# Kernel optimization log

Measured on AMD Instinct MI355X. Metric: run time of the kernel, lower is better.

## Reference

```python
import jax, jax.numpy as jnp
import numpy as np

D = 1024
EPS = 1e-5

def layer_norm(x, g, b):
    m = jnp.mean(x, axis=-1, keepdims=True)
    v = jnp.mean(jnp.square(x - m), axis=-1, keepdims=True)
    return (x - m) * jax.lax.rsqrt(v + EPS) * g + b

def setup_inputs() -> dict:
    key = jax.random.key(0)
    ks = jax.random.split(key, 8)
    S, B = 4096, 4
    s = 1.0 / np.sqrt(D)
    return {
        "x": jax.random.normal(ks[0], (S, B, D), dtype=jnp.float32),
        "W_v": jax.random.uniform(ks[1], (D, D), jnp.float32, -s, s),
        "theta": jax.random.uniform(ks[2], (D, D), jnp.float32, -s, s),
        "ln1_g": jnp.ones((D,), jnp.float32),
        "ln1_b": jnp.zeros((D,), jnp.float32),
        "ln2_g": jnp.ones((D,), jnp.float32),
        "ln2_b": jnp.zeros((D,), jnp.float32),
        "w1": jax.random.uniform(ks[3], (4 * D, D), jnp.float32, -s, s),
        "b1": jnp.zeros((4 * D,), jnp.float32),
        "w2": jax.random.uniform(ks[4], (D, 4 * D), jnp.float32, -1.0 / np.sqrt(4 * D), 1.0 / np.sqrt(4 * D)),
        "b2": jnp.zeros((D,), jnp.float32),
    }

def reference(x, W_v, theta, ln1_g, ln1_b, ln2_g, ln2_b, w1, b1, w2, b2):
    # x: [S, B, D]
    h = layer_norm(x, ln1_g, ln1_b)
    X = jnp.transpose(h, (1, 0, 2))          # [B, n, D], n = S
    n = X.shape[1]
    XWv = X @ W_v.T                          # [B, n, D]
    Xth = X @ theta.T                        # [B, n, D]
    # first term: (1/n) * ones(n,n) @ XWv == seq-mean broadcast over rows
    first = jnp.mean(XWv, axis=1, keepdims=True)
    # second term reassociated: (X @ theta(X)^T) @ XWv == X @ (theta(X)^T @ XWv)
    M = jnp.einsum('bnd,bne->bde', Xth, XWv)  # [B, D, D]
    second = (1.0 / (n * np.sqrt(D))) * jnp.einsum('bnd,bde->bne', X, M)
    attn = first + second                    # [B, n, D]
    X = X + attn
    h = jnp.transpose(X, (1, 0, 2))          # [S, B, D]
    h2 = layer_norm(h, ln2_g, ln2_b)
    mlp = jax.nn.gelu(h2 @ w1.T + b1, approximate=False) @ w2.T + b2
    return h + mlp
```

## Files before the change

kernel.cpp:

```cpp
#include <hip/hip_runtime.h>
#include <math.h>

#define S_ 4096
#define B_ 4
#define D_ 1024
#define R_ (S_*B_)
#define H_ (4*D_)

typedef unsigned short u16;
typedef unsigned int   u32;
typedef __attribute__((ext_vector_type(8))) short bf16x8;
typedef __attribute__((ext_vector_type(4))) float f32x4;

__device__ __forceinline__ u16 f2bf(float f) {
  u32 u = __float_as_uint(f);
  u32 r = (u + 0x7fffu + ((u >> 16) & 1u)) >> 16;
  return (u16)r;
}
__device__ __forceinline__ float bf2f(u16 u) {
  return __uint_as_float(((u32)u) << 16);
}

__device__ __forceinline__ void gl_lds16(const u16* g, u16* l) {
  __builtin_amdgcn_global_load_lds((const __attribute__((address_space(1))) void*)g,
                                   (__attribute__((address_space(3))) void*)l,
                                   16, 0, 0);
}
__device__ __forceinline__ void BAR() {
  asm volatile("s_barrier" ::: "memory");
}

__device__ __forceinline__ float gelu_f(float t) {
  const float u2 = 1.5957691216f * t + 0.0713548162726f * t * t * t;
  return t / (1.0f + __expf(-u2));
}

__global__ __launch_bounds__(256) void f2bf_k(const float* __restrict__ in,
                                              u16* __restrict__ out, int n4) {
  int i = blockIdx.x * 256 + threadIdx.x;
  if (i < n4) {
    float4 v = ((const float4*)in)[i];
    ushort4 o = make_ushort4(f2bf(v.x), f2bf(v.y), f2bf(v.z), f2bf(v.w));
    ((ushort4*)out)[i] = o;
  }
}

template<bool TR>
__global__ __launch_bounds__(256) void ln_k(const float* __restrict__ x,
                                            u16* __restrict__ o,
                                            const float* __restrict__ g,
                                            const float* __restrict__ bb) {
  const int row = blockIdx.x;
  const int tid = threadIdx.x;
  const float4 v = *(const float4*)&x[(long)row * D_ + tid * 4];
  float vv[4] = {v.x, v.y, v.z, v.w};
  float s = vv[0] + vv[1] + vv[2] + vv[3];
  float q = vv[0]*vv[0] + vv[1]*vv[1] + vv[2]*vv[2] + vv[3]*vv[3];
  const int l = tid & 63, w = tid >> 6;
  #pragma unroll
  for (int off = 32; off > 0; off >>= 1) {
    s += __shfl_down(s, off, 64);
    q += __shfl_down(q, off, 64);
  }
  __shared__ float red[8];
  if (l == 0) { red[w] = s; red[4 + w] = q; }
  __syncthreads();
  s = red[0] + red[1] + red[2] + red[3];
  q = red[4] + red[5] + red[6] + red[7];
  const float m   = s * (1.0f / D_);
  const float var = q * (1.0f / D_) - m * m;
  const float inv = rsqrtf(var + 1e-5f);
  const long orow = TR ? ((long)(row % B_) * S_ + (row / B_)) : (long)row;
  const int j = tid * 4;
  ushort4 ou = make_ushort4(
      f2bf((vv[0] - m) * inv * g[j+0] + bb[j+0]),
      f2bf((vv[1] - m) * inv * g[j+1] + bb[j+1]),
      f2bf((vv[2] - m) * inv * g[j+2] + bb[j+2]),
      f2bf((vv[3] - m) * inv * g[j+3] + bb[j+3]));
  *(ushort4*)&o[orow * D_ + j] = ou;
}

__global__ __launch_bounds__(256) void colsum_k(const u16* __restrict__ Xw,
                                                float* __restrict__ first) {
  const int d  = blockIdx.x * 256 + threadIdx.x;
  const int b  = blockIdx.z;
  const int n0 = blockIdx.y * 256;
  const u16* p = Xw + ((long)b * S_ + n0) * D_ + d;
  float s = 0.f;
  #pragma unroll 8
  for (int n = 0; n < 256; ++n) s += bf2f(p[(long)n * D_]);
  atomicAdd(&first[b * D_ + d], s);
}

__global__ __launch_bounds__(256) void tr_k(const u16* __restrict__ in,
                                            u16* __restrict__ out) {
  __shared__ u16 t[64][65];
  const int b  = blockIdx.z;
  const int e0 = blockIdx.x * 64;
  const int n0 = blockIdx.y * 64;
  const int tid = threadIdx.x;
  #pragma unroll
  for (int i = 0; i < 4; ++i) {
    const int v = i * 256 + tid;
    const int r = v >> 4;
    const int c = (v & 15) << 2;
    ushort4 d4 = *(const ushort4*)&in[((long)b * S_ + n0 + r) * D_ + e0 + c];
    t[r][c+0] = d4.x; t[r][c+1] = d4.y; t[r][c+2] = d4.z; t[r][c+3] = d4.w;
  }
  __syncthreads();
  #pragma unroll
  for (int i = 0; i < 4; ++i) {
    const int v = i * 256 + tid;
    const int e = v >> 4;
    const int c = (v & 15) << 2;
    ushort4 o4 = make_ushort4(t[c+0][e], t[c+1][e], t[c+2][e], t[c+3][e]);
    *(ushort4*)&out[((long)b * D_ + e0 + e) * S_ + n0 + c] = o4;
  }
}

template<int EPI>
__global__ __launch_bounds__(256, 2) void gemm_k(
    const u16* __restrict__ A, long sAz,
    const u16* __restrict__ B, long sBz,
    int K, int ldc,
    u16* __restrict__ Cb, long sCz,
    float* __restrict__ Cf,
    const float* __restrict__ vec1,
    float scale)
{
  const int bz = blockIdx.z;
  const u16* Ab = A + (long)bz * sAz;
  const u16* Bb = B + (long)bz * sBz;
  const int row0 = blockIdx.x * 128;
  const int col0 = blockIdx.y * 128;
  const int lda = K;

  __shared__ __align__(16) u16 As[128 * 32];
  __shared__ __align__(16) u16 Bs[128 * 32];

  const int tid = threadIdx.x;
  const int w = tid >> 6;
  const int l = tid & 63;
  const int wr = (w >> 1) * 64;
  const int wc = (w & 1) * 64;

  f32x4 acc[4][4];
  #pragma unroll
  for (int mi = 0; mi < 4; ++mi)
    #pragma unroll
    for (int ni = 0; ni < 4; ++ni) acc[mi][ni] = (f32x4){0.f, 0.f, 0.f, 0.f};

  const int lrow = l & 15;
  const int lo   = l >> 4;

  for (int k0 = 0; k0 < K; k0 += 32) {
    __syncthreads();
    #pragma unroll
    for (int it = 0; it < 2; ++it) {
      const int cb = it * 256 + (w << 6);
      const int c  = cb + l;
      const int r  = c >> 2;
      const int qs = ((c & 3) ^ ((r >> 1) & 3)) << 3;
      gl_lds16(Ab + (long)(row0 + r) * lda + (k0 + qs), &As[cb << 3]);
      gl_lds16(Bb + (long)(col0 + r) * lda + (k0 + qs), &Bs[cb << 3]);
    }
    __syncthreads();

    bf16x8 af[4], bfr[4];
    #pragma unroll
    for (int mi = 0; mi < 4; ++mi) {
      const int R = wr + mi * 16 + lrow;
      af[mi]  = *(const bf16x8*)&As[R * 32 + ((lo ^ ((R >> 1) & 3)) << 3)];
    }
    #pragma unroll
    for (int ni = 0; ni < 4; ++ni) {
      const int R = wc + ni * 16 + lrow;
      bfr[ni] = *(const bf16x8*)&Bs[R * 32 + ((lo ^ ((R >> 1) & 3)) << 3)];
    }
    #pragma unroll
    for (int mi = 0; mi < 4; ++mi)
      #pragma unroll
      for (int ni = 0; ni < 4; ++ni)
        acc[mi][ni] = __builtin_amdgcn_mfma_f32_16x16x32_bf16(af[mi], bfr[ni], acc[mi][ni], 0, 0, 0);
  }

  const int rbase = row0 + wr + (lo << 2);
  const int cbase = col0 + wc + lrow;
  #pragma unroll
  for (int mi = 0; mi < 4; ++mi)
    #pragma unroll
    for (int ni = 0; ni < 4; ++ni)
      #pragma unroll
      for (int r = 0; r < 4; ++r) {
        const int i = rbase + mi * 16 + r;
        const int j = cbase + ni * 16;
        if constexpr (EPI == 0)
          Cb[(long)bz * sCz + (long)i * ldc + j] = f2bf(acc[mi][ni][r]);
      }
  (void)Cf; (void)vec1; (void)scale;
}

template<int EPI>
__global__ __launch_bounds__(512, 2) void gemm256_k(
    const u16* __restrict__ A, long sAz,
    const u16* __restrict__ B, long sBz,
    int K, int ldc,
    u16* __restrict__ Cb, long sCz,
    float* __restrict__ Cf,
    const float* __restrict__ vec1,
    float scale)
{
  const int bz = blockIdx.z;
  const u16* Ab = A + (long)bz * sAz;
  const u16* Bb = B + (long)bz * sBz;
  const int row0 = blockIdx.x * 256;
  const int col0 = blockIdx.y * 256;

  __shared__ __align__(16) u16 Lds[2][2][2][256 * 32];

  const int tid = threadIdx.x;
  const int w   = tid >> 6;
  const int l   = tid & 63;
  const int wm  = w >> 2;
  const int wn  = w & 3;
  const int lr  = l & 15;
  const int lo  = l >> 4;

  const int NKH = K >> 5;
  const int NT  = K >> 6;

  const int rs   = w * 32 + (l >> 2);
  const int qsrc = ((l & 3) ^ ((l >> 3) & 3)) << 3;

  const int qsw = (lo ^ ((lr >> 1) & 3)) << 3;

  auto STAGE = [&](int khg, int op) {
    if (khg >= NKH) return;
    const u16* src = (op ? Bb : Ab) + (long)((op ? col0 : row0) + rs) * K + khg * 32 + qsrc;
    u16* dst = &Lds[(khg >> 1) & 1][khg & 1][op][(w * 2) * 512];
    gl_lds16(src, dst);
    gl_lds16(src + (long)16 * K, dst + 512);
  };

  f32x4 acc[8][4];
  #pragma unroll
  for (int mi = 0; mi < 8; ++mi)
    #pragma unroll
    for (int ni = 0; ni < 4; ++ni) acc[mi][ni] = (f32x4){0.f, 0.f, 0.f, 0.f};

  STAGE(0, 0); STAGE(0, 1);
  STAGE(1, 0); STAGE(1, 1);
  STAGE(2, 0); STAGE(2, 1);
  asm volatile("s_waitcnt vmcnt(8)" ::: "memory");
  BAR();

  for (int kt = 0; kt < NT; ++kt) {
    const u16* L00 = &Lds[kt & 1][0][0][0];
    const u16* L01 = &Lds[kt & 1][0][1][0];
    const u16* L10 = &Lds[kt & 1][1][0][0];
    const u16* L11 = &Lds[kt & 1][1][1][0];
    bf16x8 af[4], bf[4];

    #pragma unroll
    for (int ni = 0; ni < 4; ++ni)
      bf[ni] = *(const bf16x8*)&L01[(wn * 64 + ni * 16 + lr) * 32 + qsw];
    #pragma unroll
    for (int mi = 0; mi < 4; ++mi)
      af[mi] = *(const bf16x8*)&L00[(wm * 128 + mi * 16 + lr) * 32 + qsw];
    STAGE(2 * kt + 3, 0);
    BAR();
    __builtin_amdgcn_s_setprio(1);
    #pragma unroll
    for (int mi = 0; mi < 4; ++mi)
      #pragma unroll
      for (int ni = 0; ni < 4; ++ni)
        acc[mi][ni] = __builtin_amdgcn_mfma_f32_16x16x32_bf16(af[mi], bf[ni], acc[mi][ni], 0, 0, 0);
    __builtin_amdgcn_s_setprio(0);
    BAR();

    #pragma unroll
    for (int mi = 0; mi < 4; ++mi)
      af[mi] = *(const bf16x8*)&L00[(wm * 128 + 64 + mi * 16 + lr) * 32 + qsw];
    STAGE(2 * kt + 3, 1);
    if (kt == NT - 1) asm volatile("s_waitcnt vmcnt(0)" ::: "memory");
    else              asm volatile("s_waitcnt vmcnt(8)" ::: "memory");
    BAR();
    __builtin_amdgcn_s_setprio(1);
    #pragma unroll
    for (int mi = 0; mi < 4; ++mi)
      #pragma unroll
      for (int ni = 0; ni < 4; ++ni)
        acc[4 + mi][ni] = __builtin_amdgcn_mfma_f32_16x16x32_bf16(af[mi], bf[ni], acc[4 + mi][ni], 0, 0, 0);
    __builtin_amdgcn_s_setprio(0);
    BAR();

    #pragma unroll
    for (int ni = 0; ni < 4; ++ni)
      bf[ni] = *(const bf16x8*)&L11[(wn * 64 + ni * 16 + lr) * 32 + qsw];
    #pragma unroll
    for (int mi = 0; mi < 4; ++mi)
      af[mi] = *(const bf16x8*)&L10[(wm * 128 + mi * 16 + lr) * 32 + qsw];
    STAGE(2 * kt + 4, 0);
    BAR();
    __builtin_amdgcn_s_setprio(1);
    #pragma unroll
    for (int mi = 0; mi < 4; ++mi)
      #pragma unroll
      for (int ni = 0; ni < 4; ++ni)
        acc[mi][ni] = __builtin_amdgcn_mfma_f32_16x16x32_bf16(af[mi], bf[ni], acc[mi][ni], 0, 0, 0);
    __builtin_amdgcn_s_setprio(0);
    BAR();

    #pragma unroll
    for (int mi = 0; mi < 4; ++mi)
      af[mi] = *(const bf16x8*)&L10[(wm * 128 + 64 + mi * 16 + lr) * 32 + qsw];
    STAGE(2 * kt + 4, 1);
    if (kt < NT - 2)       asm volatile("s_waitcnt vmcnt(8)" ::: "memory");
    else if (kt == NT - 2) asm volatile("s_waitcnt vmcnt(4)" ::: "memory");
    else                   asm volatile("s_waitcnt vmcnt(0)" ::: "memory");
    BAR();
    __builtin_amdgcn_s_setprio(1);
    #pragma unroll
    for (int mi = 0; mi < 4; ++mi)
      #pragma unroll
      for (int ni = 0; ni < 4; ++ni)
        acc[4 + mi][ni] = __builtin_amdgcn_mfma_f32_16x16x32_bf16(af[mi], bf[ni], acc[4 + mi][ni], 0, 0, 0);
    __builtin_amdgcn_s_setprio(0);
    BAR();
  }

  {
    float* E = (float*)(&Lds[0][0][0][0]);
    const int wbase = w * (32 * 72);
    #pragma unroll
    for (int p = 0; p < 4; ++p) {
      #pragma unroll
      for (int mh = 0; mh < 2; ++mh) {
        const int a = ((p >> 1) << 2) + ((p & 1) << 1) + mh;
        #pragma unroll
        for (int ni = 0; ni < 4; ++ni)
          #pragma unroll
          for (int r = 0; r < 4; ++r)
            E[wbase + (mh * 16 + lo * 4 + r) * 72 + ni * 16 + lr] = acc[a][ni][r];
      }
      #pragma unroll
      for (int rr = 0; rr < 8; ++rr) {
        const int rl = (l >> 4) + rr * 4;
        const int cl = (l & 15) * 4;
        const f32x4 v = *(const f32x4*)&E[wbase + rl * 72 + cl];
        const long i = row0 + wm * 128 + p * 32 + rl;
        const int  j = col0 + wn * 64 + cl;
        if constexpr (EPI == 0) {
          ushort4 o = make_ushort4(f2bf(v[0]), f2bf(v[1]), f2bf(v[2]), f2bf(v[3]));
          *(ushort4*)&Cb[(long)bz * sCz + i * ldc + j] = o;
        } else if constexpr (EPI == 1) {
          const ushort4 xv = *(const ushort4*)&Ab[i * K + j];
          const f32x4 f1 = *(const f32x4*)&vec1[bz * D_ + j];
          f32x4 o;
          o[0] = bf2f(xv.x) + f1[0] * (1.0f / S_) + scale * v[0];
          o[1] = bf2f(xv.y) + f1[1] * (1.0f / S_) + scale * v[1];
          o[2] = bf2f(xv.z) + f1[2] * (1.0f / S_) + scale * v[2];
          o[3] = bf2f(xv.w) + f1[3] * (1.0f / S_) + scale * v[3];
          *(f32x4*)&Cf[(i * B_ + bz) * (long)D_ + j] = o;
        } else if constexpr (EPI == 2) {
          const f32x4 b = *(const f32x4*)&vec1[j];
          ushort4 o = make_ushort4(f2bf(gelu_f(v[0] + b[0])),
                                   f2bf(gelu_f(v[1] + b[1])),
                                   f2bf(gelu_f(v[2] + b[2])),
                                   f2bf(gelu_f(v[3] + b[3])));
          *(ushort4*)&Cb[i * ldc + j] = o;
        } else {
          const f32x4 b = *(const f32x4*)&vec1[j];
          f32x4 c = *(const f32x4*)&Cf[i * ldc + j];
          c[0] += v[0] + b[0]; c[1] += v[1] + b[1];
          c[2] += v[2] + b[2]; c[3] += v[3] + b[3];
          *(f32x4*)&Cf[i * ldc + j] = c;
        }
      }
    }
  }
}

extern "C" void kernel_launch(void* const* d_in, const int* in_sizes, int n_in,
                              void* d_out, int out_size, void* d_ws, size_t ws_size,
                              hipStream_t stream) {
  (void)in_sizes; (void)n_in; (void)out_size; (void)ws_size;
  const float* x     = (const float*)d_in[0];
  const float* W_v   = (const float*)d_in[1];
  const float* theta = (const float*)d_in[2];
  const float* ln1g  = (const float*)d_in[3];
  const float* ln1b  = (const float*)d_in[4];
  const float* ln2g  = (const float*)d_in[5];
  const float* ln2b  = (const float*)d_in[6];
  const float* w1    = (const float*)d_in[7];
  const float* b1    = (const float*)d_in[8];
  const float* w2    = (const float*)d_in[9];
  const float* b2    = (const float*)d_in[10];
  float* out = (float*)d_out;

  char* ws = (char*)d_ws;
  const size_t MB = 1024ull * 1024ull;
  u16*   Wv_bf = (u16*)(ws + 0);
  u16*   Th_bf = (u16*)(ws + 2 * MB);
  u16*   w1_bf = (u16*)(ws + 4 * MB);
  u16*   w2_bf = (u16*)(ws + 12 * MB);
  float* first = (float*)(ws + 20 * MB);
  u16*   Mt    = (u16*)(ws + 21 * MB);
  u16*   Xn    = (u16*)(ws + 29 * MB);
  u16*   XWv   = (u16*)(ws + 61 * MB);
  u16*   Xth   = (u16*)(ws + 93 * MB);
  u16*   XWvT  = (u16*)(ws + 125 * MB);
  u16*   XthT  = (u16*)(ws + 157 * MB);
  u16*   h2    = (u16*)(ws + 29 * MB);
  u16*   G     = (u16*)(ws + 61 * MB);

  f2bf_k<<<dim3((D_*D_/4 + 255)/256), 256, 0, stream>>>(W_v,   Wv_bf, D_*D_/4);
  f2bf_k<<<dim3((D_*D_/4 + 255)/256), 256, 0, stream>>>(theta, Th_bf, D_*D_/4);
  f2bf_k<<<dim3((H_*D_/4 + 255)/256), 256, 0, stream>>>(w1,    w1_bf, H_*D_/4);
  f2bf_k<<<dim3((H_*D_/4 + 255)/256), 256, 0, stream>>>(w2,    w2_bf, H_*D_/4);

  ln_k<true><<<dim3(R_), 256, 0, stream>>>(x, Xn, ln1g, ln1b);

  gemm256_k<0><<<dim3(R_/256, D_/256, 2), 512, 0, stream>>>(
      Xn, 0, Wv_bf, (long)D_*D_, D_, D_, XWv, (long)R_*D_, nullptr, nullptr, 0.f);

  hipMemsetAsync(first, 0, B_ * D_ * sizeof(float), stream);
  colsum_k<<<dim3(D_/256, 16, B_), 256, 0, stream>>>(XWv, first);

  tr_k<<<dim3(D_/64, S_/64, B_), 256, 0, stream>>>(XWv, XWvT);
  tr_k<<<dim3(D_/64, S_/64, B_), 256, 0, stream>>>(Xth, XthT);

  gemm_k<0><<<dim3(D_/128, D_/128, B_), 256, 0, stream>>>(
      XWvT, (long)D_*S_, XthT, (long)D_*S_, S_, D_, Mt, (long)D_*D_, nullptr, nullptr, 0.f);

  gemm256_k<1><<<dim3(S_/256, D_/256, B_), 512, 0, stream>>>(
      Xn, (long)S_*D_, Mt, (long)D_*D_, D_, D_, nullptr, 0, out, first,
      1.0f / ((float)S_ * 32.0f));

  ln_k<false><<<dim3(R_), 256, 0, stream>>>(out, h2, ln2g, ln2b);

  gemm256_k<2><<<dim3(R_/256, H_/256, 1), 512, 0, stream>>>(
      h2, 0, w1_bf, 0, D_, H_, G, 0, nullptr, b1, 0.f);
  gemm256_k<3><<<dim3(R_/256, D_/256, 1), 512, 0, stream>>>(
      G, 0, w2_bf, 0, H_, D_, nullptr, 0, out, b2, 0.f);
}
```

Baseline: 600.0 us.

## Fuse column-sum and transpose into the XWv/Xth projection GEMM epilogue

Adds an EPI==4 epilogue to the 256-tile GEMM that reduces accumulator columns into the sequence-mean buffer with atomics and writes the output transposed through LDS. This removes the separate colsum kernel and two transpose kernels along with the round trip of the XWv/Xth intermediates through global memory. The cost is a heavier epilogue with strided transposed stores of 16-byte chunks and atomic adds, and the colsum now uses fp32 accumulators before bf16 rounding.

```diff
diff --git a/kernel.cpp b/kernel.cpp
--- a/kernel.cpp
+++ b/kernel.cpp
@@ -80,44 +80,6 @@
   *(ushort4*)&o[orow * D_ + j] = ou;
 }
 
-__global__ __launch_bounds__(256) void colsum_k(const u16* __restrict__ Xw,
-                                                float* __restrict__ first) {
-  const int d  = blockIdx.x * 256 + threadIdx.x;
-  const int b  = blockIdx.z;
-  const int n0 = blockIdx.y * 256;
-  const u16* p = Xw + ((long)b * S_ + n0) * D_ + d;
-  float s = 0.f;
-  #pragma unroll 8
-  for (int n = 0; n < 256; ++n) s += bf2f(p[(long)n * D_]);
-  atomicAdd(&first[b * D_ + d], s);
-}
-
-__global__ __launch_bounds__(256) void tr_k(const u16* __restrict__ in,
-                                            u16* __restrict__ out) {
-  __shared__ u16 t[64][65];
-  const int b  = blockIdx.z;
-  const int e0 = blockIdx.x * 64;
-  const int n0 = blockIdx.y * 64;
-  const int tid = threadIdx.x;
-  #pragma unroll
-  for (int i = 0; i < 4; ++i) {
-    const int v = i * 256 + tid;
-    const int r = v >> 4;
-    const int c = (v & 15) << 2;
-    ushort4 d4 = *(const ushort4*)&in[((long)b * S_ + n0 + r) * D_ + e0 + c];
-    t[r][c+0] = d4.x; t[r][c+1] = d4.y; t[r][c+2] = d4.z; t[r][c+3] = d4.w;
-  }
-  __syncthreads();
-  #pragma unroll
-  for (int i = 0; i < 4; ++i) {
-    const int v = i * 256 + tid;
-    const int e = v >> 4;
-    const int c = (v & 15) << 2;
-    ushort4 o4 = make_ushort4(t[c+0][e], t[c+1][e], t[c+2][e], t[c+3][e]);
-    *(ushort4*)&out[((long)b * D_ + e0 + e) * S_ + n0 + c] = o4;
-  }
-}
-
 template<int EPI>
 __global__ __launch_bounds__(256, 2) void gemm_k(
     const u16* __restrict__ A, long sAz,
@@ -329,7 +291,45 @@
     BAR();
   }
 
-  {
+  if constexpr (EPI == 4) {
+    const int b = row0 / S_;
+    if (bz == 0) {
+      #pragma unroll
+      for (int ni = 0; ni < 4; ++ni) {
+        float s = 0.f;
+        #pragma unroll
+        for (int a = 0; a < 8; ++a)
+          #pragma unroll
+          for (int r = 0; r < 4; ++r) s += acc[a][ni][r];
+        s += __shfl_down(s, 16, 64);
+        s += __shfl_down(s, 32, 64);
+        if (lo == 0) atomicAdd(&Cf[b * D_ + (col0 + wn * 64 + ni * 16 + lr)], s);
+      }
+    }
+    u16* Tw = ((u16*)Lds) + w * (64 * 68);
+    u16* dst = Cb + (long)bz * sCz + (long)b * D_ * S_;
+    const long ib0 = (row0 % S_) + wm * 128;
+    #pragma unroll
+    for (int p = 0; p < 2; ++p) {
+      #pragma unroll
+      for (int mi = 0; mi < 4; ++mi) {
+        const int a = p * 4 + mi;
+        #pragma unroll
+        for (int ni = 0; ni < 4; ++ni) {
+          ushort4 pk = make_ushort4(f2bf(acc[a][ni][0]), f2bf(acc[a][ni][1]),
+                                    f2bf(acc[a][ni][2]), f2bf(acc[a][ni][3]));
+          *(ushort4*)&Tw[(ni * 16 + lr) * 68 + mi * 16 + lo * 4] = pk;
+        }
+      }
+      #pragma unroll
+      for (int it = 0; it < 8; ++it) {
+        const int jj = it * 8 + (l >> 3);
+        const int ic = (l & 7) * 8;
+        bf16x8 v = *(const bf16x8*)&Tw[jj * 68 + ic];
+        *(bf16x8*)&dst[(long)(col0 + wn * 64 + jj) * S_ + (ib0 + p * 64 + ic)] = v;
+      }
+    }
+  } else {
     float* E = (float*)(&Lds[0][0][0][0]);
     const int wbase = w * (32 * 72);
     #pragma unroll
@@ -407,10 +407,8 @@
   float* first = (float*)(ws + 20 * MB);
   u16*   Mt    = (u16*)(ws + 21 * MB);
   u16*   Xn    = (u16*)(ws + 29 * MB);
-  u16*   XWv   = (u16*)(ws + 61 * MB);
-  u16*   Xth   = (u16*)(ws + 93 * MB);
-  u16*   XWvT  = (u16*)(ws + 125 * MB);
-  u16*   XthT  = (u16*)(ws + 157 * MB);
+  u16*   XWvT  = (u16*)(ws + 61 * MB);
+  u16*   XthT  = (u16*)(ws + 93 * MB);
   u16*   h2    = (u16*)(ws + 29 * MB);
   u16*   G     = (u16*)(ws + 61 * MB);
 
@@ -421,14 +419,10 @@
 
   ln_k<true><<<dim3(R_), 256, 0, stream>>>(x, Xn, ln1g, ln1b);
 
-  gemm256_k<0><<<dim3(R_/256, D_/256, 2), 512, 0, stream>>>(
-      Xn, 0, Wv_bf, (long)D_*D_, D_, D_, XWv, (long)R_*D_, nullptr, nullptr, 0.f);
-
   hipMemsetAsync(first, 0, B_ * D_ * sizeof(float), stream);
-  colsum_k<<<dim3(D_/256, 16, B_), 256, 0, stream>>>(XWv, first);
-
-  tr_k<<<dim3(D_/64, S_/64, B_), 256, 0, stream>>>(XWv, XWvT);
-  tr_k<<<dim3(D_/64, S_/64, B_), 256, 0, stream>>>(Xth, XthT);
+  gemm256_k<4><<<dim3(R_/256, D_/256, 2), 512, 0, stream>>>(
+      Xn, 0, Wv_bf, (long)D_*D_, D_, D_,
+      XWvT, (long)D_*S_*B_, first, nullptr, 0.f);
 
   gemm_k<0><<<dim3(D_/128, D_/128, B_), 256, 0, stream>>>(
       XWvT, (long)D_*S_, XthT, (long)D_*S_, S_, D_, Mt, (long)D_*D_, nullptr, nullptr, 0.f);
```

Result: faster. 566.4 us (-5.6%).
